# Performance work log

Hardware: AMD Instinct MI355X
Metric: run time of the kernel (lower is better)

The kernel has to match this reference:

```python
import jax, jax.numpy as jnp
import numpy as np

# SLAYER neuron / simulation parameters (from netParams)
THETA = 10.0      # spike threshold
TAU_SR = 10.0     # synaptic (psp) alpha-kernel time constant
TAU_REF = 1.0     # refractory alpha-kernel time constant
SCALE_REF = 2.0   # refractory kernel scale
TS = 1.0          # simulation time step

N, C, H, W_SP, T = 8, 2, 50, 63, 500
OUT = 128


def _alpha_scan(x_t_first, tau, gain):
    """Causal convolution with alpha kernel k[dt] = gain*(dt*TS/tau)*exp(1-dt*TS/tau),
    k[0]=0, expressed as an exact 2-state linear recursion (O(T) instead of O(T^2)).
    x_t_first: [T, ...]. Returns [T, ...]."""
    r = jnp.exp(jnp.asarray(-TS / tau, x_t_first.dtype))
    c = jnp.asarray(gain * (TS / tau) * np.e, x_t_first.dtype)

    def step(carry, xt):
        A, B = carry          # A = sum c*dt*r^dt, B = sum c*r^dt over past inputs
        out = A               # kernel is 0 at dt=0, so x[t] does not contribute yet
        Bp = B + c * xt
        return (r * (A + Bp), r * Bp), out

    zeros = jnp.zeros_like(x_t_first[0])
    _, out = jax.lax.scan(step, (zeros, zeros), x_t_first)
    return out


def _spike_scan(u_t_first):
    """SLAYER getSpikes: sequential threshold with refractory alpha kernel
    nu[dt] = -SCALE_REF*THETA*(dt*TS/TAU_REF)*exp(1-dt*TS/TAU_REF).
    u_t_first: [T, N, O] membrane input. Returns spikes [T, N, O]."""
    r = jnp.exp(jnp.asarray(-TS / TAU_REF, u_t_first.dtype))
    c = jnp.asarray(-SCALE_REF * THETA * (TS / TAU_REF) * np.e, u_t_first.dtype)

    def step(carry, ut):
        A, B = carry
        u = ut + A                       # membrane + accumulated refractory response
        s = (u >= THETA).astype(u.dtype)
        Bp = B + c * s
        return (r * (A + Bp), r * Bp), s

    zeros = jnp.zeros_like(u_t_first[0])
    _, s = jax.lax.scan(step, (zeros, zeros), u_t_first)
    return s


def setup_inputs() -> dict:
    key = jax.random.key(0)
    k1, k2 = jax.random.split(key)
    downsampled = (jax.random.uniform(k1, (N, C, H, W_SP, T)) < 0.05).astype(jnp.float32)
    W = jax.random.normal(k2, (OUT, C * H * W_SP), dtype=jnp.float32) * 0.05
    return {"downsampled": downsampled, "W": W}


def reference(downsampled, W):
    # psp: alpha-kernel temporal filter over every input element
    x = jnp.moveaxis(downsampled, -1, 0)            # [T, N, C, H, W]
    a = _alpha_scan(x, TAU_SR, 1.0)                  # [T, N, C, H, W]
    # dense: full-spatial projection per time step
    a = a.reshape(T, N, C * H * W_SP)                # [T, N, CHW]
    u = jnp.einsum('tnc,oc->tno', a, W)              # [T, N, OUT]
    # spike generation with refractory dynamics
    s = _spike_scan(u)                               # [T, N, OUT]
    s = jnp.moveaxis(s, 0, -1)                       # [N, OUT, T]
    return s.reshape(N, OUT, 1, 1, T)                # SLAYER dense output layout
```

## Files before the change

### kernel.cpp

```cpp
#include <hip/hip_runtime.h>

#define NB 8
#define CHW 6300
#define TT 500
#define OUT 128
#define NO 1024
#define NK32 200
#define KSPLIT 8
#define NKC (NK32/KSPLIT)

typedef __attribute__((ext_vector_type(8))) _Float16 f16x8;
typedef __attribute__((ext_vector_type(4))) float f32x4;

__device__ __forceinline__ void wg_barrier_lgkm() {
    asm volatile("s_waitcnt lgkmcnt(0)" ::: "memory");
    __builtin_amdgcn_s_barrier();
}

__global__ __launch_bounds__(512) void packW(const float* __restrict__ W,
                                             _Float16* __restrict__ Wp) {
    const int tid = threadIdx.x;
    const int osub = tid >> 6;
    const int lane = tid & 63;
    const int k32 = blockIdx.x;
    const int hl = blockIdx.y;
    const int o = osub * 16 + (lane & 15);
    const int cb = k32 * 32 + (lane >> 4) * 8;

    union { _Float16 h[8]; uint4 u; } tmp;
#pragma unroll
    for (int i = 0; i < 8; i++) {
        int c = cb + i;
        float w = (c < CHW) ? W[(size_t)o * CHW + c] : 0.f;
        _Float16 hi = (_Float16)w;
        tmp.h[i] = (hl == 0) ? hi : (_Float16)((w - (float)hi) * 2048.f);
    }
    size_t lr = (((size_t)hl * NK32 + k32) * 8 + osub) * 64 + lane;
    *(uint4*)(Wp + lr * 8) = tmp.u;
}

__global__ __launch_bounds__(256, 2) void gemm(const float* __restrict__ x,
                                               const _Float16* __restrict__ Wp,
                                               float* __restrict__ vp) {
    const int L = blockIdx.x;
    const int logical = (L & 7) * 64 + (L >> 3);
    const int tb = logical & 7;
    const int n  = (logical >> 3) & 7;
    const int ks = logical >> 6;

    const int tid = threadIdx.x;
    const int wave = tid >> 6;
    const int lane = tid & 63;
    const int l15 = lane & 15;
    const int lg  = lane >> 4;
    const int rr  = lg;
    const int ch  = l15;
    const int k32_0 = ks * NKC;

    __shared__ float    Ls[2][32][65];
    __shared__ _Float16 Bs[2][4][512];

    const float* xn = x + (size_t)n * CHW * TT;
    const int toff = tb * 64 + ch * 4;
    const bool tbok = (tb < 7);

    f32x4 acc[2][4][2] = {};
    f16x8 Ar0[2][2], Ar1[2][2];
    float4 sA[2], sB[2];
    const float4 f4z = make_float4(0.f, 0.f, 0.f, 0.f);

#define XG(set, it)                                                                \
    {                                                                              \
        _Pragma("unroll") for (int p = 0; p < 2; p++) {                            \
            const int r_ = wave * 8 + p * 4 + rr;                                  \
            const int c_ = (k32_0 + (it)) * 32 + r_;                               \
            const bool v_ = (c_ < CHW) && (tbok || ch < 13);                       \
            set[p] = v_ ? *(const float4*)(xn + (size_t)c_ * TT + toff) : f4z;     \
        }                                                                          \
    }

#define DSW(set, bufL)                                                             \
    {                                                                              \
        _Pragma("unroll") for (int p = 0; p < 2; p++) {                            \
            const int r_ = wave * 8 + p * 4 + rr;                                  \
            Ls[bufL][r_][ch * 4 + 0] = set[p].x;                                   \
            Ls[bufL][r_][ch * 4 + 1] = set[p].y;                                   \
            Ls[bufL][r_][ch * 4 + 2] = set[p].z;                                   \
            Ls[bufL][r_][ch * 4 + 3] = set[p].w;                                   \
        }                                                                          \
    }

#define TRANS(bufL, bufB)                                                          \
    {                                                                              \
        float tv_[8];                                                              \
        _Pragma("unroll") for (int i = 0; i < 8; i++)                              \
            tv_[i] = Ls[bufL][lg * 8 + i][wave * 16 + l15];                        \
        union { _Float16 h[8]; uint4 u; } tc_;                                     \
        _Pragma("unroll") for (int i = 0; i < 8; i++)                              \
            tc_.h[i] = (_Float16)tv_[i];                                           \
        *(uint4*)&Bs[bufB][wave][lane * 8] = tc_.u;                                \
    }

#define ALOAD(Ar, it)                                                              \
    _Pragma("unroll") for (int of = 0; of < 2; of++)                               \
        _Pragma("unroll") for (int hl = 0; hl < 2; hl++)                           \
            Ar[of][hl] = *(const f16x8*)(Wp +                                      \
                ((((size_t)hl * NK32 + k32_0 + (it)) * 8 + wave * 2 + of) * 64 +   \
                 lane) * 8);

#define COMPUTE(buf, Ar)                                                           \
    {                                                                              \
        f16x8 bfr[4];                                                              \
        _Pragma("unroll") for (int tf = 0; tf < 4; tf++)                           \
            bfr[tf] = *(const f16x8*)&Bs[buf][tf][lane * 8];                       \
        _Pragma("unroll") for (int of = 0; of < 2; of++)                           \
            _Pragma("unroll") for (int tf = 0; tf < 4; tf++)                       \
                _Pragma("unroll") for (int hl = 0; hl < 2; hl++)                   \
                    acc[of][tf][hl] = __builtin_amdgcn_mfma_f32_16x16x32_f16(      \
                        Ar[of][hl], bfr[tf], acc[of][tf][hl], 0, 0, 0);            \
    }

    XG(sA, 0)
    XG(sB, 1)
    DSW(sA, 0)
    XG(sA, 2)
    wg_barrier_lgkm();
    TRANS(0, 0)
    DSW(sB, 1)
    XG(sB, 3)
    ALOAD(Ar0, 0)
    wg_barrier_lgkm();

    for (int p = 0; p < 12; ++p) {
        const int it = 2 * p;
        ALOAD(Ar1, it + 1)
        DSW(sA, 0)
        if (p <= 10) { XG(sA, it + 4) }
        TRANS(1, 1)
        COMPUTE(0, Ar0)
        wg_barrier_lgkm();
        ALOAD(Ar0, it + 2)
        if (p <= 10) { DSW(sB, 1) }
        if (p <= 9)  { XG(sB, it + 5) }
        TRANS(0, 0)
        COMPUTE(1, Ar1)
        wg_barrier_lgkm();
    }
    COMPUTE(0, Ar0)

    const float inv = 1.f / 2048.f;
#pragma unroll
    for (int of = 0; of < 2; of++) {
        const int o0 = (wave * 2 + of) * 16 + lg * 4;
#pragma unroll
        for (int tf = 0; tf < 4; tf++) {
            const int t = tb * 64 + tf * 16 + l15;
            if (t < TT) {
                f32x4 vo;
#pragma unroll
                for (int r = 0; r < 4; r++)
                    vo[r] = acc[of][tf][0][r] + acc[of][tf][1][r] * inv;
                *(f32x4*)(vp + (((size_t)ks * TT + t) * NB + n) * OUT + o0) = vo;
            }
        }
    }
#undef XG
#undef DSW
#undef TRANS
#undef ALOAD
#undef COMPUTE
}

__global__ __launch_bounds__(256) void reduceK(const float* __restrict__ vp,
                                               float* __restrict__ vred) {
    int i = blockIdx.x * 256 + threadIdx.x;
    const float4* p = (const float4*)vp;
    float4 a = p[i];
#pragma unroll
    for (int k = 1; k < KSPLIT; k++) {
        float4 b = p[(size_t)k * (TT * NO / 4) + i];
        a.x += b.x; a.y += b.y; a.z += b.z; a.w += b.w;
    }
    ((float4*)vred)[i] = a;
}

#define SCN_RA 0.9048374180359595f
#define SCN_RACA 0.24596031111569496f
#define SCN_RS 0.36787944117144233f
#define SCN_RSCS -20.0f
#define SCN_RSCS2 -40.0f
#define SCN_RSRSCS -7.3575888234288467f
#define SCN_TH 10.0f

#define CHAIN_STEP(i)                                                   \
    {                                                                   \
        float ua = Aa;                                                  \
        float w = fmaf(SCN_RS, G, ua);                                  \
        float u = sp ? (w + SCN_RSCS) : w;                              \
        bool sn = (u >= SCN_TH);                                        \
        sbuf[i][lane] = sn ? 1.f : 0.f;                                 \
        float Gb = fmaf(SCN_RS, G, H);                                  \
        G = sp ? (Gb + SCN_RSCS2) : Gb;                                 \
        float Hb = SCN_RS * H;                                          \
        H = sp ? (Hb + SCN_RSRSCS) : Hb;                                \
        sp = sn;                                                        \
        Ba = fmaf(SCN_RA, Ba, SCN_RACA * vv[i]);                        \
        Aa = fmaf(SCN_RA, Aa, Ba);                                      \
    }

__global__ __launch_bounds__(512) void scanspike(const float* __restrict__ vred,
                                                 float* __restrict__ out) {
    const int tid = threadIdx.x;
    const int wave = tid >> 6;
    const int lane = tid & 63;
    const int g0 = blockIdx.x * 64;

    __shared__ float vbuf[2][64][64];
    __shared__ float sbuf[64][65];

    for (int r = wave; r < 64; r += 8)
        vbuf[0][r][lane] = vred[(size_t)r * NO + g0 + lane];
    __syncthreads();

    float Aa = 0.f, Ba = 0.f, G = 0.f, H = 0.f;
    bool sp = false;

    for (int tb = 0; tb < 8; ++tb) {
        const int cur = tb & 1;
        const int t0 = tb * 64;
        const int cnt = (tb == 7) ? 52 : 64;

        if (wave == 0) {
            if (cnt == 64) {
                float vv[64];
#pragma unroll
                for (int i = 0; i < 64; ++i) vv[i] = vbuf[cur][i][lane];
#pragma unroll
                for (int i = 0; i < 64; ++i) CHAIN_STEP(i)
            } else {
                float vv[52];
#pragma unroll
                for (int i = 0; i < 52; ++i) vv[i] = vbuf[cur][i][lane];
#pragma unroll
                for (int i = 0; i < 52; ++i) CHAIN_STEP(i)
            }
        } else if (tb < 7) {
            const int nt0 = t0 + 64;
            const int ncnt = (tb == 6) ? 52 : 64;
            for (int r = wave - 1; r < ncnt; r += 7)
                vbuf[cur ^ 1][r][lane] = vred[(size_t)(nt0 + r) * NO + g0 + lane];
        }
        __syncthreads();

#pragma unroll
        for (int j = 0; j < 8; ++j) {
            int r = wave * 8 + j;
            int gr = g0 + r;
            int nn = gr >> 7;
            int oo = gr & 127;
            if (lane < cnt)
                out[((size_t)nn * OUT + oo) * TT + t0 + lane] = sbuf[lane][r];
        }
        __syncthreads();
    }
}

extern "C" void kernel_launch(void* const* d_in, const int* in_sizes, int n_in,
                              void* d_out, int out_size, void* d_ws, size_t ws_size,
                              hipStream_t stream) {
    const float* x = (const float*)d_in[0];
    const float* W = (const float*)d_in[1];
    float* out = (float*)d_out;

    _Float16* Wp   = (_Float16*)d_ws;
    float*    vp   = (float*)((char*)d_ws + 3276800);
    float*    vred = (float*)((char*)d_ws + 3276800 + 16384000);

    packW<<<dim3(NK32, 2), 512, 0, stream>>>(W, Wp);
    gemm<<<512, 256, 0, stream>>>(x, Wp, vp);
    reduceK<<<TT * NO / 4 / 256, 256, 0, stream>>>(vp, vred);
    scanspike<<<16, 512, 0, stream>>>(vred, out);
}
```

Measured before the change: 58.33 us.

## Fuse weight packing into GEMM and split-K reduction into spike scan

Removes the packW kernel: the GEMM now loads fp32 weights straight from W and splits them into hi/lo fp16 parts in registers. Removes the reduceK kernel: scanspike sums the eight split-K partials as it loads them, and now runs 32 blocks of 32 channels each. This drops two launches and the round trip of the packed-weight and reduced buffers through memory. In exchange the GEMM does more scattered fp32 weight loads plus conversion work in its inner loop, and only half of wave 0 runs the sequential scan.

```diff
diff --git a/kernel.cpp b/kernel.cpp
--- a/kernel.cpp
+++ b/kernel.cpp
@@ -17,30 +17,8 @@
     __builtin_amdgcn_s_barrier();
 }
 
-__global__ __launch_bounds__(512) void packW(const float* __restrict__ W,
-                                             _Float16* __restrict__ Wp) {
-    const int tid = threadIdx.x;
-    const int osub = tid >> 6;
-    const int lane = tid & 63;
-    const int k32 = blockIdx.x;
-    const int hl = blockIdx.y;
-    const int o = osub * 16 + (lane & 15);
-    const int cb = k32 * 32 + (lane >> 4) * 8;
-
-    union { _Float16 h[8]; uint4 u; } tmp;
-#pragma unroll
-    for (int i = 0; i < 8; i++) {
-        int c = cb + i;
-        float w = (c < CHW) ? W[(size_t)o * CHW + c] : 0.f;
-        _Float16 hi = (_Float16)w;
-        tmp.h[i] = (hl == 0) ? hi : (_Float16)((w - (float)hi) * 2048.f);
-    }
-    size_t lr = (((size_t)hl * NK32 + k32) * 8 + osub) * 64 + lane;
-    *(uint4*)(Wp + lr * 8) = tmp.u;
-}
-
 __global__ __launch_bounds__(256, 2) void gemm(const float* __restrict__ x,
-                                               const _Float16* __restrict__ Wp,
+                                               const float* __restrict__ W,
                                                float* __restrict__ vp) {
     const int L = blockIdx.x;
     const int logical = (L & 7) * 64 + (L >> 3);
@@ -71,22 +49,22 @@
 
 #define XG(set, it)                                                                \
     {                                                                              \
-        _Pragma("unroll") for (int p = 0; p < 2; p++) {                            \
-            const int r_ = wave * 8 + p * 4 + rr;                                  \
+        _Pragma("unroll") for (int p_ = 0; p_ < 2; p_++) {                         \
+            const int r_ = wave * 8 + p_ * 4 + rr;                                 \
             const int c_ = (k32_0 + (it)) * 32 + r_;                               \
             const bool v_ = (c_ < CHW) && (tbok || ch < 13);                       \
-            set[p] = v_ ? *(const float4*)(xn + (size_t)c_ * TT + toff) : f4z;     \
+            set[p_] = v_ ? *(const float4*)(xn + (size_t)c_ * TT + toff) : f4z;    \
         }                                                                          \
     }
 
 #define DSW(set, bufL)                                                             \
     {                                                                              \
-        _Pragma("unroll") for (int p = 0; p < 2; p++) {                            \
-            const int r_ = wave * 8 + p * 4 + rr;                                  \
-            Ls[bufL][r_][ch * 4 + 0] = set[p].x;                                   \
-            Ls[bufL][r_][ch * 4 + 1] = set[p].y;                                   \
-            Ls[bufL][r_][ch * 4 + 2] = set[p].z;                                   \
-            Ls[bufL][r_][ch * 4 + 3] = set[p].w;                                   \
+        _Pragma("unroll") for (int p_ = 0; p_ < 2; p_++) {                         \
+            const int r_ = wave * 8 + p_ * 4 + rr;                                 \
+            Ls[bufL][r_][ch * 4 + 0] = set[p_].x;                                  \
+            Ls[bufL][r_][ch * 4 + 1] = set[p_].y;                                  \
+            Ls[bufL][r_][ch * 4 + 2] = set[p_].z;                                  \
+            Ls[bufL][r_][ch * 4 + 3] = set[p_].w;                                  \
         }                                                                          \
     }
 
@@ -101,12 +79,32 @@
         *(uint4*)&Bs[bufB][wave][lane * 8] = tc_.u;                                \
     }
 
-#define ALOAD(Ar, it)                                                              \
-    _Pragma("unroll") for (int of = 0; of < 2; of++)                               \
-        _Pragma("unroll") for (int hl = 0; hl < 2; hl++)                           \
-            Ar[of][hl] = *(const f16x8*)(Wp +                                      \
-                ((((size_t)hl * NK32 + k32_0 + (it)) * 8 + wave * 2 + of) * 64 +   \
-                 lane) * 8);
+#define WLOAD(Ar, it)                                                              \
+    {                                                                              \
+        const int c_ = (k32_0 + (it)) * 32 + lg * 8;                               \
+        _Pragma("unroll") for (int of = 0; of < 2; of++) {                         \
+            const int o_ = (wave * 2 + of) * 16 + l15;                             \
+            const float* wp_ = W + (size_t)o_ * CHW + c_;                          \
+            float wv_[8];                                                          \
+            if (c_ + 8 <= CHW) {                                                   \
+                float4 a_ = *(const float4*)(wp_);                                 \
+                float4 b_ = *(const float4*)(wp_ + 4);                             \
+                wv_[0] = a_.x; wv_[1] = a_.y; wv_[2] = a_.z; wv_[3] = a_.w;        \
+                wv_[4] = b_.x; wv_[5] = b_.y; wv_[6] = b_.z; wv_[7] = b_.w;        \
+            } else {                                                               \
+                _Pragma("unroll") for (int i = 0; i < 8; i++)                      \
+                    wv_[i] = (c_ + i < CHW) ? wp_[i] : 0.f;                        \
+            }                                                                      \
+            union { _Float16 h[8]; f16x8 v; } hi_, lo_;                            \
+            _Pragma("unroll") for (int i = 0; i < 8; i++) {                        \
+                _Float16 h_ = (_Float16)wv_[i];                                    \
+                hi_.h[i] = h_;                                                     \
+                lo_.h[i] = (_Float16)((wv_[i] - (float)h_) * 2048.f);              \
+            }                                                                      \
+            Ar[of][0] = hi_.v;                                                     \
+            Ar[of][1] = lo_.v;                                                     \
+        }                                                                          \
+    }
 
 #define COMPUTE(buf, Ar)                                                           \
     {                                                                              \
@@ -128,18 +126,18 @@
     TRANS(0, 0)
     DSW(sB, 1)
     XG(sB, 3)
-    ALOAD(Ar0, 0)
+    WLOAD(Ar0, 0)
     wg_barrier_lgkm();
 
     for (int p = 0; p < 12; ++p) {
         const int it = 2 * p;
-        ALOAD(Ar1, it + 1)
+        WLOAD(Ar1, it + 1)
         DSW(sA, 0)
         if (p <= 10) { XG(sA, it + 4) }
         TRANS(1, 1)
         COMPUTE(0, Ar0)
         wg_barrier_lgkm();
-        ALOAD(Ar0, it + 2)
+        WLOAD(Ar0, it + 2)
         if (p <= 10) { DSW(sB, 1) }
         if (p <= 9)  { XG(sB, it + 5) }
         TRANS(0, 0)
@@ -167,21 +165,8 @@
 #undef XG
 #undef DSW
 #undef TRANS
-#undef ALOAD
+#undef WLOAD
 #undef COMPUTE
-}
-
-__global__ __launch_bounds__(256) void reduceK(const float* __restrict__ vp,
-                                               float* __restrict__ vred) {
-    int i = blockIdx.x * 256 + threadIdx.x;
-    const float4* p = (const float4*)vp;
-    float4 a = p[i];
-#pragma unroll
-    for (int k = 1; k < KSPLIT; k++) {
-        float4 b = p[(size_t)k * (TT * NO / 4) + i];
-        a.x += b.x; a.y += b.y; a.z += b.z; a.w += b.w;
-    }
-    ((float4*)vred)[i] = a;
 }
 
 #define SCN_RA 0.9048374180359595f
@@ -208,18 +193,28 @@
         Aa = fmaf(SCN_RA, Aa, Ba);                                      \
     }
 
-__global__ __launch_bounds__(512) void scanspike(const float* __restrict__ vred,
+__global__ __launch_bounds__(512) void scanspike(const float* __restrict__ vp,
                                                  float* __restrict__ out) {
     const int tid = threadIdx.x;
     const int wave = tid >> 6;
     const int lane = tid & 63;
-    const int g0 = blockIdx.x * 64;
-
-    __shared__ float vbuf[2][64][64];
-    __shared__ float sbuf[64][65];
-
-    for (int r = wave; r < 64; r += 8)
-        vbuf[0][r][lane] = vred[(size_t)r * NO + g0 + lane];
+    const int l5 = lane & 31;
+    const int rh = lane >> 5;
+    const int g0 = blockIdx.x * 32;
+    const int cn = g0 >> 7;
+    const int co = (g0 & 127) + l5;
+
+    __shared__ float vbuf[2][64][32];
+    __shared__ float sbuf[64][33];
+
+    for (int rp = wave; rp * 2 < 64; rp += 8) {
+        int r = rp * 2 + rh;
+        float a = 0.f;
+#pragma unroll
+        for (int k = 0; k < KSPLIT; k++)
+            a += vp[(((size_t)k * TT + r) * NB + cn) * OUT + co];
+        vbuf[0][r][l5] = a;
+    }
     __syncthreads();
 
     float Aa = 0.f, Ba = 0.f, G = 0.f, H = 0.f;
@@ -231,35 +226,41 @@
         const int cnt = (tb == 7) ? 52 : 64;
 
         if (wave == 0) {
-            if (cnt == 64) {
-                float vv[64];
-#pragma unroll
-                for (int i = 0; i < 64; ++i) vv[i] = vbuf[cur][i][lane];
-#pragma unroll
-                for (int i = 0; i < 64; ++i) CHAIN_STEP(i)
-            } else {
-                float vv[52];
-#pragma unroll
-                for (int i = 0; i < 52; ++i) vv[i] = vbuf[cur][i][lane];
-#pragma unroll
-                for (int i = 0; i < 52; ++i) CHAIN_STEP(i)
+            if (lane < 32) {
+                if (cnt == 64) {
+                    float vv[64];
+#pragma unroll
+                    for (int i = 0; i < 64; ++i) vv[i] = vbuf[cur][i][l5];
+#pragma unroll
+                    for (int i = 0; i < 64; ++i) CHAIN_STEP(i)
+                } else {
+                    float vv[52];
+#pragma unroll
+                    for (int i = 0; i < 52; ++i) vv[i] = vbuf[cur][i][l5];
+#pragma unroll
+                    for (int i = 0; i < 52; ++i) CHAIN_STEP(i)
+                }
             }
         } else if (tb < 7) {
             const int nt0 = t0 + 64;
             const int ncnt = (tb == 6) ? 52 : 64;
-            for (int r = wave - 1; r < ncnt; r += 7)
-                vbuf[cur ^ 1][r][lane] = vred[(size_t)(nt0 + r) * NO + g0 + lane];
+            for (int rp = wave - 1; rp * 2 < ncnt; rp += 7) {
+                int r = rp * 2 + rh;
+                float a = 0.f;
+#pragma unroll
+                for (int k = 0; k < KSPLIT; k++)
+                    a += vp[(((size_t)k * TT + nt0 + r) * NB + cn) * OUT + co];
+                vbuf[cur ^ 1][r][l5] = a;
+            }
         }
         __syncthreads();
 
 #pragma unroll
-        for (int j = 0; j < 8; ++j) {
-            int r = wave * 8 + j;
-            int gr = g0 + r;
-            int nn = gr >> 7;
-            int oo = gr & 127;
+        for (int j = 0; j < 4; ++j) {
+            int cc = wave * 4 + j;
+            int oo = (g0 & 127) + cc;
             if (lane < cnt)
-                out[((size_t)nn * OUT + oo) * TT + t0 + lane] = sbuf[lane][r];
+                out[((size_t)cn * OUT + oo) * TT + t0 + lane] = sbuf[lane][cc];
         }
         __syncthreads();
     }
@@ -272,12 +273,8 @@
     const float* W = (const float*)d_in[1];
     float* out = (float*)d_out;
 
-    _Float16* Wp   = (_Float16*)d_ws;
-    float*    vp   = (float*)((char*)d_ws + 3276800);
-    float*    vred = (float*)((char*)d_ws + 3276800 + 16384000);
-
-    packW<<<dim3(NK32, 2), 512, 0, stream>>>(W, Wp);
-    gemm<<<512, 256, 0, stream>>>(x, Wp, vp);
-    reduceK<<<TT * NO / 4 / 256, 256, 0, stream>>>(vp, vred);
-    scanspike<<<16, 512, 0, stream>>>(vred, out);
-}
+    float* vp = (float*)d_ws;
+
+    gemm<<<512, 256, 0, stream>>>(x, W, vp);
+    scanspike<<<32, 512, 0, stream>>>(vp, out);
+}
```

Result: slower. 62.46 us (+7.1%).
